# Kernel tuning notes

Hardware: AMD Instinct MI355X
Metric: run time of the kernel (lower is better)

The kernel has to match this reference:

```python
import math
import jax, jax.numpy as jnp
import numpy as np

D_MODEL = 1024
N_HEADS = 16
HEAD_DIM = D_MODEL // N_HEADS
FEATURE_DIM = 16
WINDOW = 64
EPS_NORM = 1e-6
EPS_DEN = 1e-6

_TRIU_I, _TRIU_J = np.triu_indices(FEATURE_DIM)

def taylor_feature_map(x):
    # x: [B,T,H,f] -> [B,T,H,1+f+f(f+1)/2]
    B, T, H, d = x.shape
    ones = jnp.ones((B, T, H, 1), dtype=x.dtype)
    outer = jnp.einsum('bthd,bthe->bthde', x, x)
    scale = jnp.full((d, d), 1.0 / math.sqrt(2), dtype=x.dtype)
    scale = scale.at[jnp.arange(d), jnp.arange(d)].set(0.5)
    outer = outer * scale
    quadratic = outer[..., _TRIU_I, _TRIU_J]
    return jnp.concatenate([ones, x, quadratic], axis=-1)

def rmsnorm(x, w):
    var = jnp.mean(x * x, axis=-1, keepdims=True)
    return x * jax.lax.rsqrt(var + EPS_NORM) * w

def setup_inputs() -> dict:
    key = jax.random.key(0)
    ks = jax.random.split(key, 9)
    B, T = 2, 2048
    std = 0.02
    return {
        'x': jax.random.normal(ks[0], (B, T, D_MODEL), jnp.float32),
        'encoder_out': jax.random.normal(ks[1], (B, T, D_MODEL), jnp.float32),
        'norm_w': jnp.ones((D_MODEL,), jnp.float32),
        'Wq': jax.random.normal(ks[2], (D_MODEL, D_MODEL), jnp.float32) * std,
        'Wkv': jax.random.normal(ks[3], (D_MODEL, 2 * D_MODEL), jnp.float32) * std,
        'Wqf': jax.random.normal(ks[4], (HEAD_DIM, FEATURE_DIM), jnp.float32) * std,
        'Wkf': jax.random.normal(ks[5], (HEAD_DIM, FEATURE_DIM), jnp.float32) * std,
        'Wwin': jax.random.normal(ks[6], (D_MODEL, 2 * D_MODEL), jnp.float32) * std,
        'Wout': jax.random.normal(ks[7], (2 * D_MODEL, D_MODEL), jnp.float32) * std,
    }

def _forward(x, encoder_out, norm_w, Wq, Wkv, Wqf, Wkf, Wwin, Wout):
    residual = x
    xn = rmsnorm(x, norm_w)
    B, T_dec, _ = xn.shape
    T_enc = encoder_out.shape[1]
    H, hd = N_HEADS, HEAD_DIM

    q = (xn @ Wq).reshape(B, T_dec, H, hd)
    kv = (encoder_out @ Wkv).reshape(B, T_enc, 2, H, hd)
    k, v = kv[:, :, 0], kv[:, :, 1]

    # Taylor linear cross-attention
    q_phi = taylor_feature_map(q @ Wqf)   # [B,T_dec,H,F]
    k_phi = taylor_feature_map(k @ Wkf)   # [B,T_enc,H,F]
    kv_state = jnp.einsum('bshf,bshd->bhfd', k_phi, v)
    k_state = k_phi.sum(axis=1)           # [B,H,F]
    linear_out = jnp.einsum('bthf,bhfd->bthd', q_phi, kv_state)
    normalizer = jnp.einsum('bthf,bhf->bth', q_phi, k_state)[..., None]
    linear_out = (linear_out / (normalizer + EPS_DEN)).reshape(B, T_dec, D_MODEL)

    # Sliding-window causal self-attention (flash window_size=(WINDOW,0))
    kv_win = (xn @ Wwin).reshape(B, T_dec, 2, H, hd)
    k_win, v_win = kv_win[:, :, 0], kv_win[:, :, 1]
    scores = jnp.einsum('bthd,bshd->bhts', q, k_win) * (1.0 / math.sqrt(hd))
    i = jnp.arange(T_dec)[:, None]
    j = jnp.arange(T_dec)[None, :]
    allowed = (j <= i) & (j >= i - WINDOW)
    scores = jnp.where(allowed, scores, jnp.finfo(scores.dtype).min)
    probs = jax.nn.softmax(scores, axis=-1)
    window_out = jnp.einsum('bhts,bshd->bthd', probs, v_win).reshape(B, T_dec, D_MODEL)

    combined = jnp.concatenate([linear_out, window_out], axis=-1)
    return residual + combined @ Wout

def reference(x, encoder_out, norm_w, Wq, Wkv, Wqf, Wkf, Wwin, Wout):
    return _forward(x, encoder_out, norm_w, Wq, Wkv, Wqf, Wkf, Wwin, Wout)
```

## Files before the change

kernel.cpp:

```cpp
#include <hip/hip_runtime.h>

#define DM 1024
#define NH 16
#define HD 64
#define FD 16
#define NF 153
#define FPAD 160
#define WIN 64
#define TSEQ 2048
#define ROWS 4096
#define KSPLIT 32
#define RS2 0.70710678118654752f

typedef unsigned short u16;
typedef __attribute__((ext_vector_type(8))) short bf16x8;
typedef __attribute__((ext_vector_type(8))) unsigned short u16x8;
typedef __attribute__((ext_vector_type(4))) unsigned short u16x4;
typedef __attribute__((ext_vector_type(4))) float f32x4;

#define GLB_AS __attribute__((address_space(1)))
#define LDS_AS __attribute__((address_space(3)))

static __device__ __forceinline__ void gload_lds16(const void* g, void* l){
  __builtin_amdgcn_global_load_lds((const GLB_AS void*)g, (LDS_AS void*)l, 16, 0, 0);
}

static __device__ __forceinline__ float bf2f(u16 u){
  unsigned v = ((unsigned)u) << 16;
  return __builtin_bit_cast(float, v);
}
static __device__ __forceinline__ u16 f2bf(float f){
  unsigned u = __builtin_bit_cast(unsigned, f);
  u += 0x7FFFu + ((u >> 16) & 1u);
  return (u16)(u >> 16);
}

static __device__ __forceinline__ void tr_tile(const float* __restrict__ in,
    u16* __restrict__ out, int K, int N, int n0, int k0, float* t, int tid){
  int tx = tid & 31, ty = tid >> 5;
  #pragma unroll
  for (int i=0;i<4;i++) t[(ty + i*8)*33 + tx] = in[(size_t)(k0 + ty + i*8)*N + n0 + tx];
  __syncthreads();
  #pragma unroll
  for (int i=0;i<4;i++) out[(size_t)(n0 + ty + i*8)*K + k0 + tx] = f2bf(t[tx*33 + ty + i*8]);
}

__global__ __launch_bounds__(256) void k_prep(const float* __restrict__ x,
    const float* __restrict__ enc, const float* __restrict__ w,
    const float* __restrict__ Wq, const float* __restrict__ Wwin,
    const float* __restrict__ Wkv, const float* __restrict__ Wout,
    const float* __restrict__ Wqf, const float* __restrict__ Wkf,
    u16* __restrict__ xn, u16* __restrict__ encb,
    u16* __restrict__ WqwT, u16* __restrict__ WkvT, u16* __restrict__ WoutT,
    u16* __restrict__ WqfT, u16* __restrict__ WkfT){
  __shared__ float t[32*33];
  int bx = blockIdx.x, tid = threadIdx.x;
  if (bx < ROWS){
    int row = bx;
    const float4* xr = (const float4*)(x + (size_t)row*DM);
    float4 a = xr[tid];
    float ss = a.x*a.x + a.y*a.y + a.z*a.z + a.w*a.w;
    #pragma unroll
    for (int m=1;m<64;m<<=1) ss += __shfl_xor(ss, m);
    __shared__ float red[4];
    if ((tid&63)==0) red[tid>>6] = ss;
    __syncthreads();
    float tot = red[0]+red[1]+red[2]+red[3];
    float rs = rsqrtf(tot*(1.0f/DM) + 1e-6f);
    float4 wv = ((const float4*)w)[tid];
    u16x4 o;
    o[0]=f2bf(a.x*rs*wv.x); o[1]=f2bf(a.y*rs*wv.y);
    o[2]=f2bf(a.z*rs*wv.z); o[3]=f2bf(a.w*rs*wv.w);
    ((u16x4*)(xn + (size_t)row*DM))[tid] = o;
  } else if (bx < 2*ROWS){
    int row = bx - ROWS;
    float4 a = ((const float4*)(enc + (size_t)row*DM))[tid];
    u16x4 o;
    o[0]=f2bf(a.x); o[1]=f2bf(a.y); o[2]=f2bf(a.z); o[3]=f2bf(a.w);
    ((u16x4*)(encb + (size_t)row*DM))[tid] = o;
  } else {
    int b = bx - 2*ROWS;
    if (b < 1024){
      tr_tile(Wq, WqwT, 1024, 1024, (b&31)*32, (b>>5)*32, t, tid);
    } else if (b < 3072){
      int r = b-1024;
      tr_tile(Wwin, WqwT + (size_t)1024*1024, 1024, 2048, (r&63)*32, (r>>6)*32, t, tid);
    } else if (b < 5120){
      int r = b-3072;
      tr_tile(Wkv, WkvT, 1024, 2048, (r&63)*32, (r>>6)*32, t, tid);
    } else if (b < 7168){
      int r = b-5120;
      tr_tile(Wout, WoutT, 2048, 1024, (r&31)*32, (r>>5)*32, t, tid);
    } else {
      const float* src = (b==7168) ? Wqf : Wkf;
      u16* dst = (b==7168) ? WqfT : WkfT;
      for (int i=tid;i<1024;i+=256) dst[i] = f2bf(src[(i&63)*16 + (i>>6)]);
    }
  }
}

template<int EPI>
__global__ __launch_bounds__(512) void k_gemm(
    const u16* __restrict__ A0, const u16* __restrict__ B0, u16* __restrict__ C0, int ldc0,
    const u16* __restrict__ A1, const u16* __restrict__ B1, u16* __restrict__ C1, int ldc1,
    int split, int K, float* __restrict__ Cf, const float* __restrict__ resid){
  __shared__ u16 As0[128*64];
  __shared__ u16 Bs0[128*64];
  __shared__ u16 As1[128*64];
  __shared__ u16 Bs1[128*64];
  int by = blockIdx.y;
  const u16 *A, *Bt; u16* C; int ldc;
  if (by < split){ A=A0; Bt=B0; C=C0; ldc=ldc0; }
  else { by -= split; A=A1; Bt=B1; C=C1; ldc=ldc1; }
  int row0 = blockIdx.x*128, col0 = by*128;
  int tid = threadIdx.x, lane = tid&63, wid = tid>>6;
  int wm = wid>>2, wn = wid&3;
  int srow = lane>>3;
  int scb  = ((lane&7)*16) ^ (srow<<4);
  f32x4 acc[4][2] = {};

  auto STAGE = [&](u16* Asb, u16* Bsb, int k0){
    #pragma unroll
    for (int i=0;i<2;i++){
      int chunk = wid*2 + i;
      int r = chunk*8 + srow;
      gload_lds16((const char*)(A  + (size_t)(row0+r)*K + k0) + scb, (char*)Asb + chunk*1024);
      gload_lds16((const char*)(Bt + (size_t)(col0+r)*K + k0) + scb, (char*)Bsb + chunk*1024);
    }
  };
  auto COMPUTE = [&](const u16* Asb, const u16* Bsb){
    #pragma unroll
    for (int kk=0;kk<64;kk+=32){
      int bc = 2*(kk + ((lane>>4)<<3));
      bf16x8 af[4], bfm[2];
      #pragma unroll
      for (int m=0;m<4;m++){
        int r = wm*64 + m*16 + (lane&15);
        af[m]  = *(const bf16x8*)((const char*)Asb + r*128 + (bc ^ ((r&7)<<4)));
      }
      #pragma unroll
      for (int n=0;n<2;n++){
        int r = wn*32 + n*16 + (lane&15);
        bfm[n] = *(const bf16x8*)((const char*)Bsb + r*128 + (bc ^ ((r&7)<<4)));
      }
      #pragma unroll
      for (int m=0;m<4;m++)
        #pragma unroll
        for (int n=0;n<2;n++)
          acc[m][n] = __builtin_amdgcn_mfma_f32_16x16x32_bf16(af[m], bfm[n], acc[m][n], 0,0,0);
    }
  };

  int nt = K >> 6;
  STAGE(As0, Bs0, 0);
  for (int t=0; t<nt-2; t+=2){
    STAGE(As1, Bs1, (t+1)*64);
    asm volatile("s_waitcnt vmcnt(4)" ::: "memory");
    __builtin_amdgcn_s_barrier();
    COMPUTE(As0, Bs0);
    __builtin_amdgcn_s_barrier();
    STAGE(As0, Bs0, (t+2)*64);
    asm volatile("s_waitcnt vmcnt(4)" ::: "memory");
    __builtin_amdgcn_s_barrier();
    COMPUTE(As1, Bs1);
    __builtin_amdgcn_s_barrier();
  }
  STAGE(As1, Bs1, (nt-1)*64);
  asm volatile("s_waitcnt vmcnt(4)" ::: "memory");
  __builtin_amdgcn_s_barrier();
  COMPUTE(As0, Bs0);
  asm volatile("s_waitcnt vmcnt(0)" ::: "memory");
  __builtin_amdgcn_s_barrier();
  COMPUTE(As1, Bs1);

  int rl = (lane>>4)<<2;
  #pragma unroll
  for (int m=0;m<4;m++){
    #pragma unroll
    for (int n=0;n<2;n++){
      int gc = col0 + wn*32 + n*16 + (lane&15);
      #pragma unroll
      for (int r=0;r<4;r++){
        size_t gi = (size_t)(row0 + wm*64 + m*16 + rl + r)*ldc + gc;
        if constexpr (EPI) Cf[gi] = acc[m][n][r] + resid[gi];
        else               C[gi]  = f2bf(acc[m][n][r]);
      }
    }
  }
}

template<int EPI>
__global__ __launch_bounds__(512) void k_gemmN64(const u16* __restrict__ A,
    const u16* __restrict__ Bt, float* __restrict__ Cf,
    const float* __restrict__ resid, int ldc, int K){
  __shared__ u16 As0[128*64];
  __shared__ u16 Bs0[64*64];
  __shared__ u16 As1[128*64];
  __shared__ u16 Bs1[64*64];
  int row0 = blockIdx.x*128, col0 = blockIdx.y*64;
  int tid = threadIdx.x, lane = tid&63, wid = tid>>6;
  int wm = wid>>1, wn = wid&1;
  int srow = lane>>3;
  int scb  = ((lane&7)*16) ^ (srow<<4);
  f32x4 acc[2][2] = {};

  auto STAGE = [&](u16* Asb, u16* Bsb, int k0){
    #pragma unroll
    for (int j=0;j<2;j++){
      int c = wid*2 + j;
      int r = c*8 + srow;
      gload_lds16((const char*)(A + (size_t)(row0+r)*K + k0) + scb, (char*)Asb + c*1024);
    }
    {
      int c = wid;
      int r = c*8 + srow;
      gload_lds16((const char*)(Bt + (size_t)(col0+r)*K + k0) + scb, (char*)Bsb + c*1024);
    }
  };
  auto COMPUTE = [&](const u16* Asb, const u16* Bsb){
    #pragma unroll
    for (int kk=0;kk<64;kk+=32){
      int bc = 2*(kk + ((lane>>4)<<3));
      bf16x8 af[2], bfm[2];
      #pragma unroll
      for (int m=0;m<2;m++){
        int r = wm*32 + m*16 + (lane&15);
        af[m]  = *(const bf16x8*)((const char*)Asb + r*128 + (bc ^ ((r&7)<<4)));
      }
      #pragma unroll
      for (int n=0;n<2;n++){
        int r = wn*32 + n*16 + (lane&15);
        bfm[n] = *(const bf16x8*)((const char*)Bsb + r*128 + (bc ^ ((r&7)<<4)));
      }
      #pragma unroll
      for (int m=0;m<2;m++)
        #pragma unroll
        for (int n=0;n<2;n++)
          acc[m][n] = __builtin_amdgcn_mfma_f32_16x16x32_bf16(af[m], bfm[n], acc[m][n], 0,0,0);
    }
  };

  int nt = K >> 6;
  STAGE(As0, Bs0, 0);
  for (int t=0; t<nt-2; t+=2){
    STAGE(As1, Bs1, (t+1)*64);
    asm volatile("s_waitcnt vmcnt(3)" ::: "memory");
    __builtin_amdgcn_s_barrier();
    COMPUTE(As0, Bs0);
    __builtin_amdgcn_s_barrier();
    STAGE(As0, Bs0, (t+2)*64);
    asm volatile("s_waitcnt vmcnt(3)" ::: "memory");
    __builtin_amdgcn_s_barrier();
    COMPUTE(As1, Bs1);
    __builtin_amdgcn_s_barrier();
  }
  STAGE(As1, Bs1, (nt-1)*64);
  asm volatile("s_waitcnt vmcnt(3)" ::: "memory");
  __builtin_amdgcn_s_barrier();
  COMPUTE(As0, Bs0);
  asm volatile("s_waitcnt vmcnt(0)" ::: "memory");
  __builtin_amdgcn_s_barrier();
  COMPUTE(As1, Bs1);

  int rl = (lane>>4)<<2;
  #pragma unroll
  for (int m=0;m<2;m++){
    #pragma unroll
    for (int n=0;n<2;n++){
      int gc = col0 + wn*32 + n*16 + (lane&15);
      #pragma unroll
      for (int r=0;r<4;r++){
        size_t gi = (size_t)(row0 + wm*32 + m*16 + rl + r)*ldc + gc;
        if constexpr (EPI) Cf[gi] = acc[m][n][r] + resid[gi];
        else               ((u16*)Cf)[gi] = f2bf(acc[m][n][r]);
      }
    }
  }
}

__global__ __launch_bounds__(256) void k_kvstate(const u16* __restrict__ kvb,
    const u16* __restrict__ WkfT, u16* __restrict__ part){
  const int P = 72;
  __shared__ u16 kc[64*64];
  __shared__ u16 wb[16*72];
  __shared__ float fL[64*16];
  __shared__ u16 ph[160*P];
  __shared__ u16 vt[80*P];
  int bh = blockIdx.x, b = bh>>4, h = bh&15;
  int ks = blockIdx.y;
  int tid = threadIdx.x, lane = tid&63, w = tid>>6;
  int srow = lane>>3;
  int scb  = ((lane&7)*16) ^ (srow<<4);
  int s0 = ks*64;
  for (int i=tid;i<1024;i+=256) wb[(i>>6)*72 + (i&63)] = WkfT[i];
  for (int i=tid; i<16*P; i+=256){
    int r = 64 + i/P, c = i - (i/P)*P;
    vt[r*P + c] = (r==64) ? (u16)0x3F80 : (u16)0;
  }
  #pragma unroll
  for (int i=0;i<2;i++){
    int ch = w + i*4;
    int r = ch*8 + srow;
    gload_lds16((const char*)(kvb + (size_t)(b*TSEQ + s0 + r)*2048 + h*HD) + scb,
                (char*)kc + ch*1024);
  }
  for (int s = w; s < 64; s += 4)
    vt[lane*P + s] = kvb[(size_t)(b*TSEQ + s0 + s)*2048 + 1024 + h*HD + lane];
  __syncthreads();
  {
    f32x4 fa = {};
    #pragma unroll
    for (int kk=0;kk<2;kk++){
      int bc = 2*(kk*32 + ((lane>>4)<<3));
      int r = w*16 + (lane&15);
      bf16x8 av = *(const bf16x8*)((const char*)kc + r*128 + (bc ^ ((r&7)<<4)));
      bf16x8 bv = *(const bf16x8*)(wb + (lane&15)*72 + kk*32 + ((lane>>4)<<3));
      fa = __builtin_amdgcn_mfma_f32_16x16x32_bf16(av, bv, fa, 0,0,0);
    }
    int rl = (lane>>4)<<2;
    #pragma unroll
    for (int r=0;r<4;r++) fL[(w*16 + rl + r)*16 + (lane&15)] = fa[r];
  }
  __syncthreads();
  {
    int r = tid>>2, jq = tid&3;
    float4 v0 = *(const float4*)(fL + r*16 + 0);
    float4 v1 = *(const float4*)(fL + r*16 + 4);
    float4 v2 = *(const float4*)(fL + r*16 + 8);
    float4 v3 = *(const float4*)(fL + r*16 + 12);
    float f[16] = {v0.x,v0.y,v0.z,v0.w, v1.x,v1.y,v1.z,v1.w,
                   v2.x,v2.y,v2.z,v2.w, v3.x,v3.y,v3.z,v3.w};
    if ((0&3)==jq) ph[0*P + r] = 0x3F80;
    #pragma unroll
    for (int q=0;q<16;q++) if (((1+q)&3)==jq) ph[(1+q)*P + r] = f2bf(f[q]);
    int pos = 17;
    #pragma unroll
    for (int i=0;i<16;i++)
      #pragma unroll
      for (int j=i;j<16;j++){
        if ((pos&3)==jq) ph[pos*P + r] = f2bf(f[i]*f[j]*((i==j)?0.5f:RS2));
        pos++;
      }
    #pragma unroll
    for (int z=153;z<160;z++) if ((z&3)==jq) ph[z*P + r] = 0;
  }
  __syncthreads();
  f32x4 acc[5][3] = {};
  #pragma unroll
  for (int kk=0;kk<2;kk++){
    int lk = kk*32 + ((lane>>4)<<3);
    bf16x8 bfr[3];
    #pragma unroll
    for (int nn=0;nn<3;nn++){
      int ncol = (nn<2) ? (w*2+nn) : (8+(w&1));
      bfr[nn] = *(const bf16x8*)(ph + (ncol*16 + (lane&15))*P + lk);
    }
    #pragma unroll
    for (int m=0;m<5;m++){
      bf16x8 av = *(const bf16x8*)(vt + (m*16 + (lane&15))*P + lk);
      #pragma unroll
      for (int nn=0;nn<3;nn++)
        acc[m][nn] = __builtin_amdgcn_mfma_f32_16x16x32_bf16(av, bfr[nn], acc[m][nn], 0,0,0);
    }
  }
  int rl = (lane>>4)<<2;
  u16* pp = part + ((size_t)ks*32 + bh)*80*160;
  #pragma unroll
  for (int m=0;m<5;m++){
    #pragma unroll
    for (int nn=0;nn<3;nn++){
      int ncol = (nn<2) ? (w*2+nn) : (8+(w&1));
      if (nn==2 && w>=2) continue;
      int fcol = ncol*16 + (lane&15);
      #pragma unroll
      for (int r=0;r<4;r++)
        pp[(size_t)(m*16 + rl + r)*160 + fcol] = f2bf(acc[m][nn][r]);
    }
  }
}

__global__ __launch_bounds__(256) void k_kvreduce(const u16* __restrict__ part,
    u16* __restrict__ kvsT){
  int i = blockIdx.x*256 + threadIdx.x;
  float s = 0.f;
  #pragma unroll
  for (int c=0;c<KSPLIT;c++) s += bf2f(part[(size_t)c*409600 + i]);
  kvsT[i] = f2bf(s);
}

__global__ __launch_bounds__(256) void k_linattn(const u16* __restrict__ qwin,
    const u16* __restrict__ WqfT, const u16* __restrict__ kvsT, u16* __restrict__ comb){
  const int LS = 168;
  __shared__ u16 As[64*LS];
  __shared__ u16 Bs[80*LS];
  __shared__ float fL[64*16];
  int bh = blockIdx.x, b = bh>>4, h = bh&15;
  int t0 = blockIdx.y*64;
  int tid = threadIdx.x, lane = tid&63, wid = tid>>6;
  for (int i=tid*8; i<80*FPAD; i+=2048){
    int r = i/FPAD, ff = i - r*FPAD;
    *(bf16x8*)(Bs + r*LS + ff) = *(const bf16x8*)(kvsT + (size_t)bh*80*FPAD + i);
  }
  {
    f32x4 fa = {};
    const u16* qrow = qwin + (size_t)(b*TSEQ + t0 + wid*16 + (lane&15))*3072 + h*HD;
    const u16* wrow = WqfT + (lane&15)*64;
    #pragma unroll
    for (int kk=0;kk<2;kk++){
      int ko = kk*32 + ((lane>>4)<<3);
      bf16x8 av = *(const bf16x8*)(qrow + ko);
      bf16x8 bv = *(const bf16x8*)(wrow + ko);
      fa = __builtin_amdgcn_mfma_f32_16x16x32_bf16(av, bv, fa, 0,0,0);
    }
    int rl = (lane>>4)<<2;
    #pragma unroll
    for (int r=0;r<4;r++) fL[(wid*16 + rl + r)*16 + (lane&15)] = fa[r];
  }
  __syncthreads();
  {
    int r = tid>>2, jq = tid&3;
    float4 v0 = *(const float4*)(fL + r*16 + 0);
    float4 v1 = *(const float4*)(fL + r*16 + 4);
    float4 v2 = *(const float4*)(fL + r*16 + 8);
    float4 v3 = *(const float4*)(fL + r*16 + 12);
    float f[16] = {v0.x,v0.y,v0.z,v0.w, v1.x,v1.y,v1.z,v1.w,
                   v2.x,v2.y,v2.z,v2.w, v3.x,v3.y,v3.z,v3.w};
    if ((0&3)==jq) As[r*LS + 0] = 0x3F80;
    #pragma unroll
    for (int q=0;q<16;q++) if (((1+q)&3)==jq) As[r*LS + 1+q] = f2bf(f[q]);
    int pos = 17;
    #pragma unroll
    for (int i=0;i<16;i++)
      #pragma unroll
      for (int j=i;j<16;j++){
        if ((pos&3)==jq) As[r*LS + pos] = f2bf(f[i]*f[j]*((i==j)?0.5f:RS2));
        pos++;
      }
    #pragma unroll
    for (int z=153;z<160;z++) if ((z&3)==jq) As[r*LS + z] = 0;
  }
  __syncthreads();
  f32x4 acc[5] = {};
  __builtin_amdgcn_s_setprio(1);
  #pragma unroll
  for (int ks=0;ks<5;ks++){
    int lk = ks*32 + ((lane>>4)<<3);
    bf16x8 a = *(const bf16x8*)(As + (wid*16 + (lane&15))*LS + lk);
    #pragma unroll
    for (int n=0;n<5;n++){
      bf16x8 bb = *(const bf16x8*)(Bs + (n*16 + (lane&15))*LS + lk);
      acc[n] = __builtin_amdgcn_mfma_f32_16x16x32_bf16(a, bb, acc[n], 0,0,0);
    }
  }
  __builtin_amdgcn_s_setprio(0);
  int rl = (lane>>4)<<2;
  #pragma unroll
  for (int r=0;r<4;r++){
    float nrm = __shfl(acc[4][r], lane & 48) + 1e-6f;
    float inv = 1.0f / nrm;
    int t = t0 + wid*16 + rl + r;
    #pragma unroll
    for (int n=0;n<4;n++){
      comb[(size_t)(b*TSEQ + t)*2048 + h*64 + n*16 + (lane&15)] = f2bf(acc[n][r]*inv);
    }
  }
}

__global__ __launch_bounds__(256) void k_window(const u16* __restrict__ qwin,
    u16* __restrict__ comb){
  const int LQ = 72, LV = 136;
  __shared__ u16 k_s [128*LQ];
  __shared__ u16 vT  [64*LV];
  __shared__ u16 p_s [64*LV];
  int bh = blockIdx.x, b = bh>>4, h = bh&15;
  int t0 = blockIdx.y*64;
  int tid = threadIdx.x, lane = tid&63, wid = tid>>6;
  int j0 = t0 - 64;
  bf16x8 zv = {0,0,0,0,0,0,0,0};
  for (int cc=tid; cc<1024; cc+=256){
    int r = cc>>3, c8 = cc&7;
    int j = j0 + r;
    bf16x8 kv8 = (j>=0) ? *(const bf16x8*)(qwin + (size_t)(b*TSEQ + j)*3072 + 1024 + h*HD + c8*8) : zv;
    *(bf16x8*)(k_s + r*LQ + c8*8) = kv8;
    bf16x8 vv8 = (j>=0) ? *(const bf16x8*)(qwin + (size_t)(b*TSEQ + j)*3072 + 2048 + h*HD + c8*8) : zv;
    int cs = r ^ (c8<<3);
    #pragma unroll
    for (int e=0;e<8;e++) vT[(c8*8+e)*LV + cs] = (u16)vv8[e];
  }
  __syncthreads();
  f32x4 sa[8] = {};
  {
    const u16* qrow = qwin + (size_t)(b*TSEQ + t0 + wid*16 + (lane&15))*3072 + h*HD;
    __builtin_amdgcn_s_setprio(1);
    #pragma unroll
    for (int kk=0;kk<64;kk+=32){
      int lk = kk + ((lane>>4)<<3);
      bf16x8 a = *(const bf16x8*)(qrow + lk);
      #pragma unroll
      for (int n=0;n<8;n++){
        bf16x8 bb = *(const bf16x8*)(k_s + (n*16 + (lane&15))*LQ + lk);
        sa[n] = __builtin_amdgcn_mfma_f32_16x16x32_bf16(a, bb, sa[n], 0,0,0);
      }
    }
    __builtin_amdgcn_s_setprio(0);
  }
  int rl = (lane>>4)<<2;
  float pr[8][4];
  #pragma unroll
  for (int r=0;r<4;r++){
    int ig = t0 + wid*16 + rl + r;
    float mx = -1e30f;
    float sv[8];
    #pragma unroll
    for (int n=0;n<8;n++){
      int jg = j0 + n*16 + (lane&15);
      float s = sa[n][r]*0.125f;
      bool ok = (jg>=0) && (jg<=ig) && (jg>=ig-WIN);
      s = ok ? s : -1e30f;
      sv[n]=s; mx = fmaxf(mx, s);
    }
    #pragma unroll
    for (int m=1;m<16;m<<=1) mx = fmaxf(mx, __shfl_xor(mx, m));
    float sum = 0.f;
    #pragma unroll
    for (int n=0;n<8;n++){ float e = __expf(sv[n]-mx); sv[n]=e; sum += e; }
    #pragma unroll
    for (int m=1;m<16;m<<=1) sum += __shfl_xor(sum, m);
    float inv = 1.0f/sum;
    #pragma unroll
    for (int n=0;n<8;n++) pr[n][r] = sv[n]*inv;
  }
  #pragma unroll
  for (int n=0;n<8;n++)
    #pragma unroll
    for (int r=0;r<4;r++)
      p_s[(wid*16 + rl + r)*LV + n*16 + (lane&15)] = f2bf(pr[n][r]);
  __syncthreads();
  f32x4 oa[4] = {};
  __builtin_amdgcn_s_setprio(1);
  #pragma unroll
  for (int ks=0;ks<4;ks++){
    int lk = ks*32 + ((lane>>4)<<3);
    bf16x8 a = *(const bf16x8*)(p_s + (wid*16 + (lane&15))*LV + lk);
    #pragma unroll
    for (int n=0;n<4;n++){
      int d = n*16 + (lane&15);
      bf16x8 bb = *(const bf16x8*)(vT + d*LV + (lk ^ (((d>>3)&7)<<3)));
      oa[n] = __builtin_amdgcn_mfma_f32_16x16x32_bf16(a, bb, oa[n], 0,0,0);
    }
  }
  __builtin_amdgcn_s_setprio(0);
  #pragma unroll
  for (int n=0;n<4;n++)
    #pragma unroll
    for (int r=0;r<4;r++)
      comb[(size_t)(b*TSEQ + t0 + wid*16 + rl + r)*2048 + 1024 + h*HD + n*16 + (lane&15)]
        = f2bf(oa[n][r]);
}

extern "C" void kernel_launch(void* const* d_in, const int* in_sizes, int n_in,
                              void* d_out, int out_size, void* d_ws, size_t ws_size,
                              hipStream_t stream){
  (void)in_sizes; (void)n_in; (void)out_size; (void)ws_size;
  const float* x    = (const float*)d_in[0];
  const float* enc  = (const float*)d_in[1];
  const float* nw   = (const float*)d_in[2];
  const float* Wq   = (const float*)d_in[3];
  const float* Wkv  = (const float*)d_in[4];
  const float* Wqf  = (const float*)d_in[5];
  const float* Wkf  = (const float*)d_in[6];
  const float* Wwin = (const float*)d_in[7];
  const float* Wout = (const float*)d_in[8];
  float* out = (float*)d_out;

  char* p = (char*)d_ws;
  auto alloc = [&](size_t bytes)->char*{
    char* r = p; p += (bytes + 255) & ~(size_t)255; return r;
  };
  char*  aliasBase = p;
  u16*   xn    = (u16*)  alloc((size_t)ROWS*DM*2);
  u16*   encb  = (u16*)  alloc((size_t)ROWS*DM*2);
  u16*   WqwT  = (u16*)  alloc((size_t)3072*DM*2);
  u16*   WkvT  = (u16*)  alloc((size_t)2048*DM*2);
  u16*   part  = (u16*)  aliasBase;
  u16*   WoutT = (u16*)  alloc((size_t)DM*2048*2);
  u16*   WqfT  = (u16*)  alloc((size_t)FD*HD*2);
  u16*   WkfT  = (u16*)  alloc((size_t)FD*HD*2);
  u16*   qwin  = (u16*)  alloc((size_t)ROWS*3072*2);
  u16*   kvb   = (u16*)  alloc((size_t)ROWS*2048*2);
  u16*   kvsT  = (u16*)  alloc((size_t)32*80*FPAD*2);
  u16*   comb  = (u16*)  alloc((size_t)ROWS*2048*2);

  k_prep<<<2*ROWS + 7170, 256, 0, stream>>>(x, enc, nw, Wq, Wwin, Wkv, Wout, Wqf, Wkf,
                                            xn, encb, WqwT, WkvT, WoutT, WqfT, WkfT);

  k_gemm<0><<<dim3(ROWS/128, 40), 512, 0, stream>>>(
      xn, WqwT, qwin, 3072,  encb, WkvT, kvb, 2048,  24, DM, nullptr, nullptr);

  k_kvstate<<<dim3(32, KSPLIT), 256, 0, stream>>>(kvb, WkfT, part);
  k_kvreduce<<<1600, 256, 0, stream>>>(part, kvsT);

  k_linattn<<<dim3(32, TSEQ/64), 256, 0, stream>>>(qwin, WqfT, kvsT, comb);
  k_window <<<dim3(32, TSEQ/64), 256, 0, stream>>>(qwin, comb);

  k_gemmN64<1><<<dim3(ROWS/128, 16), 512, 0, stream>>>(
      comb, WoutT, out, x, DM, 2048);
}
```

Measured before the change: 158.5 us.

## Fold Wkf into the Wkv weight so the GEMM emits key features directly

Precomputes Wk·Wkf per head inside the prep kernel and replaces the K half of the encoder KV weight with this 1024x256 product. The KV GEMM output shrinks from 2048 to 1280 columns, and k_kvstate no longer loads K tiles or runs its per-block feature MFMA; it reads the 16 features straight from the GEMM output. The cost is a scalar fp32 weight-product loop in k_prep (16 blocks, 1024x16x64 each), a change in rounding order (bf16 of the fused weight), and a separate non-aliased partial buffer.

Result: slower. 202.6 us (+27.8%).

```diff
diff --git a/kernel.cpp b/kernel.cpp
--- a/kernel.cpp
+++ b/kernel.cpp
@@ -10,6 +10,7 @@
 #define TSEQ 2048
 #define ROWS 4096
 #define KSPLIT 32
+#define LDKV 1280
 #define RS2 0.70710678118654752f
 
 typedef unsigned short u16;
@@ -51,9 +52,10 @@
     const float* __restrict__ Wkv, const float* __restrict__ Wout,
     const float* __restrict__ Wqf, const float* __restrict__ Wkf,
     u16* __restrict__ xn, u16* __restrict__ encb,
-    u16* __restrict__ WqwT, u16* __restrict__ WkvT, u16* __restrict__ WoutT,
-    u16* __restrict__ WqfT, u16* __restrict__ WkfT){
+    u16* __restrict__ WqwT, u16* __restrict__ WkvT2, u16* __restrict__ WoutT,
+    u16* __restrict__ WqfT){
   __shared__ float t[32*33];
+  __shared__ float wkf[1024];
   int bx = blockIdx.x, tid = threadIdx.x;
   if (bx < ROWS){
     int row = bx;
@@ -85,16 +87,26 @@
     } else if (b < 3072){
       int r = b-1024;
       tr_tile(Wwin, WqwT + (size_t)1024*1024, 1024, 2048, (r&63)*32, (r>>6)*32, t, tid);
-    } else if (b < 5120){
+    } else if (b < 4096){
       int r = b-3072;
-      tr_tile(Wkv, WkvT, 1024, 2048, (r&63)*32, (r>>6)*32, t, tid);
-    } else if (b < 7168){
-      int r = b-5120;
+      tr_tile(Wkv + 1024, WkvT2, 1024, 2048, (r&31)*32, (r>>5)*32, t, tid);
+    } else if (b < 6144){
+      int r = b-4096;
       tr_tile(Wout, WoutT, 2048, 1024, (r&31)*32, (r>>5)*32, t, tid);
+    } else if (b == 6144){
+      for (int i=tid;i<1024;i+=256) WqfT[i] = f2bf(Wqf[(i&63)*16 + (i>>6)]);
     } else {
-      const float* src = (b==7168) ? Wqf : Wkf;
-      u16* dst = (b==7168) ? WqfT : WkfT;
-      for (int i=tid;i<1024;i+=256) dst[i] = f2bf(src[(i&63)*16 + (i>>6)]);
+      int h = b - 6145;
+      for (int i=tid;i<1024;i+=256) wkf[i] = Wkf[i];
+      __syncthreads();
+      int f = tid&15;
+      for (int din = tid>>4; din < 1024; din += 16){
+        const float* wr = Wkv + (size_t)din*2048 + h*64;
+        float acc = 0.f;
+        #pragma unroll
+        for (int d=0;d<64;d++) acc += wr[d]*wkf[d*16 + f];
+        WkvT2[(size_t)(1024 + h*16 + f)*1024 + din] = f2bf(acc);
+      }
     }
   }
 }
@@ -279,57 +291,28 @@
 }
 
 __global__ __launch_bounds__(256) void k_kvstate(const u16* __restrict__ kvb,
-    const u16* __restrict__ WkfT, u16* __restrict__ part){
+    u16* __restrict__ part){
   const int P = 72;
-  __shared__ u16 kc[64*64];
-  __shared__ u16 wb[16*72];
-  __shared__ float fL[64*16];
   __shared__ u16 ph[160*P];
   __shared__ u16 vt[80*P];
   int bh = blockIdx.x, b = bh>>4, h = bh&15;
   int ks = blockIdx.y;
   int tid = threadIdx.x, lane = tid&63, w = tid>>6;
-  int srow = lane>>3;
-  int scb  = ((lane&7)*16) ^ (srow<<4);
   int s0 = ks*64;
-  for (int i=tid;i<1024;i+=256) wb[(i>>6)*72 + (i&63)] = WkfT[i];
   for (int i=tid; i<16*P; i+=256){
     int r = 64 + i/P, c = i - (i/P)*P;
     vt[r*P + c] = (r==64) ? (u16)0x3F80 : (u16)0;
   }
-  #pragma unroll
-  for (int i=0;i<2;i++){
-    int ch = w + i*4;
-    int r = ch*8 + srow;
-    gload_lds16((const char*)(kvb + (size_t)(b*TSEQ + s0 + r)*2048 + h*HD) + scb,
-                (char*)kc + ch*1024);
-  }
   for (int s = w; s < 64; s += 4)
-    vt[lane*P + s] = kvb[(size_t)(b*TSEQ + s0 + s)*2048 + 1024 + h*HD + lane];
-  __syncthreads();
-  {
-    f32x4 fa = {};
-    #pragma unroll
-    for (int kk=0;kk<2;kk++){
-      int bc = 2*(kk*32 + ((lane>>4)<<3));
-      int r = w*16 + (lane&15);
-      bf16x8 av = *(const bf16x8*)((const char*)kc + r*128 + (bc ^ ((r&7)<<4)));
-      bf16x8 bv = *(const bf16x8*)(wb + (lane&15)*72 + kk*32 + ((lane>>4)<<3));
-      fa = __builtin_amdgcn_mfma_f32_16x16x32_bf16(av, bv, fa, 0,0,0);
-    }
-    int rl = (lane>>4)<<2;
-    #pragma unroll
-    for (int r=0;r<4;r++) fL[(w*16 + rl + r)*16 + (lane&15)] = fa[r];
-  }
-  __syncthreads();
+    vt[lane*P + s] = kvb[(size_t)(b*TSEQ + s0 + s)*LDKV + h*HD + lane];
   {
     int r = tid>>2, jq = tid&3;
-    float4 v0 = *(const float4*)(fL + r*16 + 0);
-    float4 v1 = *(const float4*)(fL + r*16 + 4);
-    float4 v2 = *(const float4*)(fL + r*16 + 8);
-    float4 v3 = *(const float4*)(fL + r*16 + 12);
-    float f[16] = {v0.x,v0.y,v0.z,v0.w, v1.x,v1.y,v1.z,v1.w,
-                   v2.x,v2.y,v2.z,v2.w, v3.x,v3.y,v3.z,v3.w};
+    const u16* kfp = kvb + (size_t)(b*TSEQ + s0 + r)*LDKV + 1024 + h*16;
+    u16x8 va = *(const u16x8*)kfp;
+    u16x8 vb = *(const u16x8*)(kfp + 8);
+    float f[16];
+    #pragma unroll
+    for (int j=0;j<8;j++){ f[j] = bf2f(va[j]); f[8+j] = bf2f(vb[j]); }
     if ((0&3)==jq) ph[0*P + r] = 0x3F80;
     #pragma unroll
     for (int q=0;q<16;q++) if (((1+q)&3)==jq) ph[(1+q)*P + r] = f2bf(f[q]);
@@ -577,27 +560,25 @@
   auto alloc = [&](size_t bytes)->char*{
     char* r = p; p += (bytes + 255) & ~(size_t)255; return r;
   };
-  char*  aliasBase = p;
   u16*   xn    = (u16*)  alloc((size_t)ROWS*DM*2);
   u16*   encb  = (u16*)  alloc((size_t)ROWS*DM*2);
   u16*   WqwT  = (u16*)  alloc((size_t)3072*DM*2);
-  u16*   WkvT  = (u16*)  alloc((size_t)2048*DM*2);
-  u16*   part  = (u16*)  aliasBase;
+  u16*   WkvT2 = (u16*)  alloc((size_t)LDKV*DM*2);
   u16*   WoutT = (u16*)  alloc((size_t)DM*2048*2);
   u16*   WqfT  = (u16*)  alloc((size_t)FD*HD*2);
-  u16*   WkfT  = (u16*)  alloc((size_t)FD*HD*2);
   u16*   qwin  = (u16*)  alloc((size_t)ROWS*3072*2);
-  u16*   kvb   = (u16*)  alloc((size_t)ROWS*2048*2);
+  u16*   kvb   = (u16*)  alloc((size_t)ROWS*LDKV*2);
   u16*   kvsT  = (u16*)  alloc((size_t)32*80*FPAD*2);
   u16*   comb  = (u16*)  alloc((size_t)ROWS*2048*2);
-
-  k_prep<<<2*ROWS + 7170, 256, 0, stream>>>(x, enc, nw, Wq, Wwin, Wkv, Wout, Wqf, Wkf,
-                                            xn, encb, WqwT, WkvT, WoutT, WqfT, WkfT);
-
-  k_gemm<0><<<dim3(ROWS/128, 40), 512, 0, stream>>>(
-      xn, WqwT, qwin, 3072,  encb, WkvT, kvb, 2048,  24, DM, nullptr, nullptr);
-
-  k_kvstate<<<dim3(32, KSPLIT), 256, 0, stream>>>(kvb, WkfT, part);
+  u16*   part  = (u16*)  alloc((size_t)KSPLIT*32*80*FPAD*2);
+
+  k_prep<<<2*ROWS + 6161, 256, 0, stream>>>(x, enc, nw, Wq, Wwin, Wkv, Wout, Wqf, Wkf,
+                                            xn, encb, WqwT, WkvT2, WoutT, WqfT);
+
+  k_gemm<0><<<dim3(ROWS/128, 34), 512, 0, stream>>>(
+      xn, WqwT, qwin, 3072,  encb, WkvT2, kvb, LDKV,  24, DM, nullptr, nullptr);
+
+  k_kvstate<<<dim3(32, KSPLIT), 256, 0, stream>>>(kvb, part);
   k_kvreduce<<<1600, 256, 0, stream>>>(part, kvsT);
 
   k_linattn<<<dim3(32, TSEQ/64), 256, 0, stream>>>(qwin, WqfT, kvsT, comb);
```
